# Kernel tuning notes

Measured on AMD Instinct MI355X. Metric: run time of the kernel, lower is better.

The kernel has to match this reference:

```python
import jax, jax.numpy as jnp
import numpy as np

# Dims: S strings, B batch, D bond dim, N=784 input sites, P=2 phys dim, L=10 labels
S, B, D, N, P, L = 4, 64, 32, 784, 2, 10
HALF = N // 2  # 392 sites on each side of the label node


def setup_inputs() -> dict:
    key = jax.random.key(0)
    ks = jax.random.split(key, 6)
    # scale chosen so each transfer-matrix step keeps vector norm ~O(1)
    std = (3.0 / (2.0 * D)) ** 0.5
    inputs = jax.random.uniform(ks[0], (B, N, P), dtype=jnp.float32)
    A_first = jax.random.normal(ks[1], (S, D, P), dtype=jnp.float32) * std          # node 0
    A_left = jax.random.normal(ks[2], (S, HALF - 1, D, P, D), dtype=jnp.float32) * std   # nodes 1..391
    A_label = jax.random.normal(ks[3], (S, D, L, D), dtype=jnp.float32) * std       # node 392 (open label edge)
    A_right = jax.random.normal(ks[4], (S, HALF - 1, D, P, D), dtype=jnp.float32) * std  # nodes 393..783
    A_last = jax.random.normal(ks[5], (S, D, P), dtype=jnp.float32) * std           # node 784
    return {"inputs": inputs, "A_first": A_first, "A_left": A_left,
            "A_label": A_label, "A_right": A_right, "A_last": A_last}


def reference(inputs, A_first, A_left, A_label, A_right, A_last):
    x = inputs  # (B, N, P); original reshapes each sample to (784, 2)
    # Contract physical legs with inputs -> per-site transfer matrices, site-major for scan
    Ml = jnp.einsum('snipj,bnp->nsbij', A_left, x[:, 1:HALF])      # (391, S, B, D, D)
    v0 = jnp.einsum('sdp,bp->sbd', A_first, x[:, 0])               # (S, B, D)

    def step_left(v, M):
        return jnp.einsum('sbi,sbij->sbj', v, M), None
    v, _ = jax.lax.scan(step_left, v0, Ml)                          # (S, B, D)

    T = jnp.einsum('sbd,sdlj->sblj', v, A_label)                    # (S, B, L, D)

    Mr = jnp.einsum('snipj,bnp->nsbij', A_right, x[:, HALF:N - 1])  # (391, S, B, D, D)
    r0 = jnp.einsum('sdp,bp->sbd', A_last, x[:, N - 1])             # (S, B, D)

    def step_right(r, M):
        return jnp.einsum('sbij,sbj->sbi', M, r), None
    r, _ = jax.lax.scan(step_right, r0, Mr, reverse=True)           # (S, B, D)

    out_per_string = jnp.einsum('sblj,sbj->sbl', T, r)              # (S, B, L)
    # forward multiplies the per-string 10-vectors elementwise (init ones)
    return jnp.prod(out_per_string, axis=0)                         # (B, L)
```

## Files before the change

kernel.cpp:

```cpp
#include <hip/hip_runtime.h>
#include <stdint.h>

#define S 4
#define B 64
#define D 32
#define N 784
#define P 2
#define L 10
#define HALF 392
#define NSTEP 391
#define NPAIR 196
#define SLICE 4096

typedef float f4 __attribute__((ext_vector_type(4)));

__device__ __forceinline__ float bcast(float v, int lane) {
    return __uint_as_float(__builtin_amdgcn_readlane(__float_as_uint(v), lane));
}

__global__ __launch_bounds__(256) void pair_kernel(
    const float* __restrict__ A_left, const float* __restrict__ A_right,
    float* __restrict__ Wbuf)
{
    const int t = blockIdx.x, stream = blockIdx.y;
    const int side = stream >> 2, s = stream & 3;
    __shared__ float sA[2048], sB[2048];
    const int tid = threadIdx.x;
    const bool leftover = (t == 195);

    const float* As = (side ? A_right : A_left) + (size_t)s * (NSTEP * 2048);
    int ia, ib;
    if (side == 0) { ia = 2 * t; ib = 2 * t + 1; }
    else           { ia = 389 - 2 * t; ib = 390 - 2 * t; }
    if (leftover)  { ia = side ? 0 : 390; ib = ia; }

    const float4* ga = (const float4*)(As + (size_t)ia * 2048);
    const float4* gb = (const float4*)(As + (size_t)ib * 2048);
    ((float4*)sA)[tid] = ga[tid]; ((float4*)sA)[tid + 256] = ga[tid + 256];
    ((float4*)sB)[tid] = gb[tid]; ((float4*)sB)[tid + 256] = gb[tid + 256];
    __syncthreads();

    const int c = tid >> 6, rest = tid & 63, ff = rest >> 1, eh = rest & 1;
    const int a = c & 1, bb = c >> 1;
    float out[16];

    if (!leftover) {
        if (side == 0) {
            float col[32];
            #pragma unroll
            for (int k = 0; k < 32; ++k) col[k] = sB[k * 64 + bb * 32 + ff];
            #pragma unroll
            for (int e0 = 0; e0 < 16; ++e0) {
                const int e = eh * 16 + e0; float acc = 0.f;
                #pragma unroll
                for (int k = 0; k < 32; ++k)
                    acc = fmaf(sA[e * 64 + a * 32 + k], col[k], acc);
                out[e0] = acc;
            }
        } else {
            float row[32];
            #pragma unroll
            for (int k = 0; k < 32; ++k) row[k] = sA[ff * 64 + a * 32 + k];
            #pragma unroll
            for (int e0 = 0; e0 < 16; ++e0) {
                const int e = eh * 16 + e0; float acc = 0.f;
                #pragma unroll
                for (int k = 0; k < 32; ++k)
                    acc = fmaf(row[k], sB[k * 64 + bb * 32 + e], acc);
                out[e0] = acc;
            }
        }
    } else {
        #pragma unroll
        for (int e0 = 0; e0 < 16; ++e0) {
            const int e = eh * 16 + e0;
            out[e0] = (side == 0) ? sA[e * 64 + a * 32 + ff]
                                  : sA[ff * 64 + a * 32 + e];
        }
    }

    float* Wt = Wbuf + ((size_t)stream * NPAIR + t) * SLICE;
    #pragma unroll
    for (int q0 = 0; q0 < 4; ++q0) {
        const int qq = eh * 4 + q0;
        float4 val = make_float4(out[q0 * 4 + 0], out[q0 * 4 + 1],
                                 out[q0 * 4 + 2], out[q0 * 4 + 3]);
        ((float4*)Wt)[(bb * 8 + qq) * 64 + a * 32 + ff] = val;
    }
}

__global__ __launch_bounds__(64) void wkern(const float* __restrict__ x,
                                            float* __restrict__ wtab)
{
    const int t = blockIdx.x, side = blockIdx.y, bb = threadIdx.x;
    const float2* x2 = (const float2*)x;
    float2 xa, xb;
    if (t < 195) {
        int na, nb;
        if (side == 0) { na = 2 * t + 1; nb = 2 * t + 2; }
        else           { int ma = 389 - 2 * t; na = HALF + ma; nb = na + 1; }
        xa = x2[(size_t)bb * N + na];
        xb = x2[(size_t)bb * N + nb];
    } else {
        const int na = side ? HALF : 391;
        xa = x2[(size_t)bb * N + na];
        xb = make_float2(1.f, 0.f);
    }
    float4 w = make_float4(xa.x * xb.x, xa.y * xb.x, xa.x * xb.y, xa.y * xb.y);
    ((float4*)wtab)[((size_t)side * NPAIR + t) * 64 + bb] = w;
}

#define GLOAD(dst, ptr, off) \
    asm volatile("global_load_dwordx4 %0, %1, off offset:" #off \
                 : "=v"(dst) : "v"(ptr))

#define ISSUE_SLOT(SL) do { \
    GLOAD(SL##0,  pA, 0); GLOAD(SL##1,  pA, 1024); GLOAD(SL##2,  pA, 2048); GLOAD(SL##3,  pA, 3072); \
    GLOAD(SL##4,  pB, 0); GLOAD(SL##5,  pB, 1024); GLOAD(SL##6,  pB, 2048); GLOAD(SL##7,  pB, 3072); \
    GLOAD(SL##8,  pC, 0); GLOAD(SL##9,  pC, 1024); GLOAD(SL##10, pC, 2048); GLOAD(SL##11, pC, 3072); \
    GLOAD(SL##12, pD, 0); GLOAD(SL##13, pD, 1024); GLOAD(SL##14, pD, 2048); GLOAD(SL##15, pD, 3072); \
    GLOAD(SL##w,  pw, 0); \
    pA += SLICE; pB += SLICE; pC += SLICE; pD += SLICE; pw += 256; \
} while (0)

#define WAIT(n) do { \
    asm volatile("s_waitcnt vmcnt(" #n ")"); \
    __builtin_amdgcn_sched_barrier(0); \
} while (0)

#define FMAQ(Rq, acc, eb) \
    acc = fmaf(Rq.x, bcast(v, eb + 0), acc); \
    acc = fmaf(Rq.y, bcast(v, eb + 1), acc); \
    acc = fmaf(Rq.z, bcast(v, eb + 2), acc); \
    acc = fmaf(Rq.w, bcast(v, eb + 3), acc);

#define CONSUME_SLOT(SL) do { \
    float a0 = 0.f, a1 = 0.f, a2 = 0.f, a3 = 0.f; \
    FMAQ(SL##0,  a0, 0)  FMAQ(SL##1,  a0, 4)  FMAQ(SL##2,  a0, 8)  FMAQ(SL##3,  a0, 12) \
    FMAQ(SL##4,  a1, 16) FMAQ(SL##5,  a1, 20) FMAQ(SL##6,  a1, 24) FMAQ(SL##7,  a1, 28) \
    FMAQ(SL##8,  a2, 0)  FMAQ(SL##9,  a2, 4)  FMAQ(SL##10, a2, 8)  FMAQ(SL##11, a2, 12) \
    FMAQ(SL##12, a3, 16) FMAQ(SL##13, a3, 20) FMAQ(SL##14, a3, 24) FMAQ(SL##15, a3, 28) \
    const float wlo = c2 ? SL##w.y : SL##w.x; \
    const float whi = c2 ? SL##w.w : SL##w.z; \
    const float part = fmaf(wlo, a0 + a1, whi * (a2 + a3)); \
    v = part + __shfl_xor(part, 32); \
} while (0)

__global__ __launch_bounds__(128, 1) void chain_kernel(
    const float* __restrict__ x,
    const float* __restrict__ A_first, const float* __restrict__ A_last,
    const float* __restrict__ Wbuf, const float* __restrict__ wtab,
    float* __restrict__ ws_v)
{
    const int tid = threadIdx.x, wv = tid >> 6, lane = tid & 63;
    const int c2 = lane >> 5, f = lane & 31;
    const int blk = blockIdx.x, stream = blk & 7;
    const int side = stream >> 2, s = stream & 3;
    const int b = (blk >> 3) * 2 + wv;

    const float2* x2 = (const float2*)x;
    float v;
    if (side == 0) {
        const float2 a  = ((const float2*)A_first)[s * D + f];
        const float2 xx = x2[(size_t)b * N + 0];
        v = fmaf(a.x, xx.x, a.y * xx.y);
    } else {
        const float2 a  = ((const float2*)A_last)[s * D + f];
        const float2 xx = x2[(size_t)b * N + (N - 1)];
        v = fmaf(a.x, xx.x, a.y * xx.y);
    }

    const float* Wstream = Wbuf + (size_t)stream * (NPAIR * SLICE);
    const float* pA = Wstream + (size_t)lane * 4;
    const float* pB = pA + 1024;
    const float* pC = pA + 2048;
    const float* pD = pA + 3072;
    const float* pw = wtab + ((size_t)side * NPAIR) * 256 + (size_t)b * 4;

    f4 A0,A1,A2,A3,A4,A5,A6,A7,A8,A9,A10,A11,A12,A13,A14,A15,Aw;
    f4 B0,B1,B2,B3,B4,B5,B6,B7,B8,B9,B10,B11,B12,B13,B14,B15,Bw;
    f4 C0,C1,C2,C3,C4,C5,C6,C7,C8,C9,C10,C11,C12,C13,C14,C15,Cw;

    ISSUE_SLOT(A);
    ISSUE_SLOT(B);

    for (int k = 0; k < 64; ++k) {
        ISSUE_SLOT(C); __builtin_amdgcn_s_barrier(); WAIT(34); CONSUME_SLOT(A);
        ISSUE_SLOT(A); __builtin_amdgcn_s_barrier(); WAIT(34); CONSUME_SLOT(B);
        ISSUE_SLOT(B); __builtin_amdgcn_s_barrier(); WAIT(34); CONSUME_SLOT(C);
    }
    ISSUE_SLOT(C);
    __builtin_amdgcn_s_barrier(); WAIT(34); CONSUME_SLOT(A);
    ISSUE_SLOT(A);
    __builtin_amdgcn_s_barrier(); WAIT(34); CONSUME_SLOT(B);
    __builtin_amdgcn_s_barrier(); WAIT(17); CONSUME_SLOT(C);
    __builtin_amdgcn_s_barrier(); WAIT(0);  CONSUME_SLOT(A);

    if (lane < 32)
        ws_v[(side * S + s) * (B * D) + b * D + f] = v;
}

__global__ __launch_bounds__(64) void chain_fb(
    const float* __restrict__ x, const float* __restrict__ A_first,
    const float* __restrict__ A_left, const float* __restrict__ A_right,
    const float* __restrict__ A_last, float* __restrict__ ws_v)
{
    const int blk = blockIdx.x, pair = blk & 7, b = blk >> 3;
    const int side = pair >> 2, s = pair & 3;
    const int lane = threadIdx.x, p = lane >> 5, j = lane & 31;
    const float* xb = x + b * (N * P);
    float v;
    if (side == 0) {
        v = fmaf(A_first[s*D*P + j*P + 0], xb[0], A_first[s*D*P + j*P + 1] * xb[1]);
        const float* Abase = A_left + (size_t)s * (NSTEP * D * P * D);
        for (int n = 1; n <= NSTEP; ++n) {
            const float* M = Abase + (n - 1) * (D * P * D) + p * D + j;
            const float x0 = xb[n*P], x1 = xb[n*P + 1];
            float t0 = 0.f, t1 = 0.f;
            #pragma unroll
            for (int i = 0; i < D; i += 2) {
                t0 = fmaf(bcast(v, i),     M[i * (P*D)],       t0);
                t1 = fmaf(bcast(v, i + 1), M[(i + 1) * (P*D)], t1);
            }
            const float t = t0 + t1, o = __shfl_xor(t, 32);
            v = (p == 0) ? fmaf(x0, t, x1 * o) : fmaf(x1, t, x0 * o);
        }
    } else {
        v = fmaf(A_last[s*D*P + j*P + 0], xb[(N-1)*P], A_last[s*D*P + j*P + 1] * xb[(N-1)*P + 1]);
        const float* Abase = A_right + (size_t)s * (NSTEP * D * P * D);
        for (int m = NSTEP - 1; m >= 0; --m) {
            const float4* R4 = (const float4*)(Abase + m * (D*P*D) + j * (P*D) + p * D);
            const float x0 = xb[(HALF+m)*P], x1 = xb[(HALF+m)*P + 1];
            float t0 = 0.f, t1 = 0.f;
            #pragma unroll
            for (int q = 0; q < 8; ++q) {
                const float4 rv = R4[q];
                t0 = fmaf(rv.x, bcast(v, 4*q+0), t0);
                t1 = fmaf(rv.y, bcast(v, 4*q+1), t1);
                t0 = fmaf(rv.z, bcast(v, 4*q+2), t0);
                t1 = fmaf(rv.w, bcast(v, 4*q+3), t1);
            }
            const float t = t0 + t1, o = __shfl_xor(t, 32);
            v = (p == 0) ? fmaf(x0, t, x1 * o) : fmaf(x1, t, x0 * o);
        }
    }
    if (p == 0) ws_v[(side*S + s)*(B*D) + b*D + j] = v;
}

__global__ __launch_bounds__(64) void label_kernel(
    const float* __restrict__ ws_v, const float* __restrict__ A_label,
    float* __restrict__ ws_o)
{
    const int blk = blockIdx.x, s = blk & 3, b = blk >> 2;
    const int lane = threadIdx.x, h = lane >> 5, j = lane & 31;
    const float vj = ws_v[(0*S + s)*(B*D) + b*D + j];
    const float rj = ws_v[(1*S + s)*(B*D) + b*D + j];
    #pragma unroll
    for (int q = 0; q < 5; ++q) {
        const int l = h * 5 + q;
        float w = 0.f;
        #pragma unroll
        for (int d = 0; d < D; ++d)
            w = fmaf(bcast(vj, d), A_label[((s*D + d)*L + l)*D + j], w);
        float c = w * rj;
        c += __shfl_xor(c, 1); c += __shfl_xor(c, 2); c += __shfl_xor(c, 4);
        c += __shfl_xor(c, 8); c += __shfl_xor(c, 16);
        if (j == 0) ws_o[(b*L + l)*S + s] = c;
    }
}

__global__ void prod_kernel(const float* __restrict__ ws_o, float* __restrict__ out) {
    const int t = blockIdx.x * blockDim.x + threadIdx.x;
    if (t < B * L) {
        const float* o = ws_o + t * S;
        out[t] = o[0] * o[1] * o[2] * o[3];
    }
}

extern "C" void kernel_launch(void* const* d_in, const int* in_sizes, int n_in,
                              void* d_out, int out_size, void* d_ws, size_t ws_size,
                              hipStream_t stream) {
    const float* x       = (const float*)d_in[0];
    const float* A_first = (const float*)d_in[1];
    const float* A_left  = (const float*)d_in[2];
    const float* A_label = (const float*)d_in[3];
    const float* A_right = (const float*)d_in[4];
    const float* A_last  = (const float*)d_in[5];
    float* out = (float*)d_out;

    float* ws_v = (float*)d_ws;
    float* ws_o = ws_v + 2 * S * B * D;
    float* wtab = ws_o + B * L * S;
    float* Wbuf = wtab + 2 * NPAIR * 64 * 4;
    const size_t need = (size_t)(16384 + 2560 + 100352 + 8 * NPAIR * SLICE) * 4;

    if (ws_size >= need) {
        pair_kernel<<<dim3(NPAIR, 8), dim3(256), 0, stream>>>(A_left, A_right, Wbuf);
        wkern<<<dim3(NPAIR, 2), dim3(64), 0, stream>>>(x, wtab);
        chain_kernel<<<dim3(256), dim3(128), 0, stream>>>(x, A_first, A_last, Wbuf, wtab, ws_v);
    } else {
        chain_fb<<<dim3(2 * S * B), dim3(64), 0, stream>>>(x, A_first, A_left, A_right, A_last, ws_v);
    }
    label_kernel<<<dim3(S * B), dim3(64), 0, stream>>>(ws_v, A_label, ws_o);
    prod_kernel<<<dim3((B * L + 255) / 256), dim3(256), 0, stream>>>(ws_o, out);
}
```

Before: 117.3 us.

## Process two batch rows per wave in chain kernel and fuse auxiliary kernels

The chain kernel now runs one 64-lane wave per block and handles two batch samples with the same loaded pair matrices, instead of two waves each loading the same data. This halves redundant global loads of the precomputed pair matrices and removes the inter-wave barriers, at the cost of more FMAs and registers per wave. The input-weight table computation moves into pair_kernel, and the label and product kernels are merged, which cuts two kernel launches.

```diff
diff --git a/kernel.cpp b/kernel.cpp
--- a/kernel.cpp
+++ b/kernel.cpp
@@ -20,10 +20,12 @@
 
 __global__ __launch_bounds__(256) void pair_kernel(
     const float* __restrict__ A_left, const float* __restrict__ A_right,
-    float* __restrict__ Wbuf)
+    const float* __restrict__ x,
+    float* __restrict__ Wbuf, float* __restrict__ wtab)
 {
-    const int t = blockIdx.x, stream = blockIdx.y;
-    const int side = stream >> 2, s = stream & 3;
+    const int stream = blockIdx.x;
+    const int t      = blockIdx.y;
+    const int side   = stream >> 2, s = stream & 3;
     __shared__ float sA[2048], sB[2048];
     const int tid = threadIdx.x;
     const bool leftover = (t == 195);
@@ -87,39 +89,36 @@
                                  out[q0 * 4 + 2], out[q0 * 4 + 3]);
         ((float4*)Wt)[(bb * 8 + qq) * 64 + a * 32 + ff] = val;
     }
-}
-
-__global__ __launch_bounds__(64) void wkern(const float* __restrict__ x,
-                                            float* __restrict__ wtab)
-{
-    const int t = blockIdx.x, side = blockIdx.y, bb = threadIdx.x;
-    const float2* x2 = (const float2*)x;
-    float2 xa, xb;
-    if (t < 195) {
-        int na, nb;
-        if (side == 0) { na = 2 * t + 1; nb = 2 * t + 2; }
-        else           { int ma = 389 - 2 * t; na = HALF + ma; nb = na + 1; }
-        xa = x2[(size_t)bb * N + na];
-        xb = x2[(size_t)bb * N + nb];
-    } else {
-        const int na = side ? HALF : 391;
-        xa = x2[(size_t)bb * N + na];
-        xb = make_float2(1.f, 0.f);
-    }
-    float4 w = make_float4(xa.x * xb.x, xa.y * xb.x, xa.x * xb.y, xa.y * xb.y);
-    ((float4*)wtab)[((size_t)side * NPAIR + t) * 64 + bb] = w;
-}
-
-#define GLOAD(dst, ptr, off) \
+
+    if (stream < 2 && tid < 64) {
+        const int sd = stream;
+        const float2* x2 = (const float2*)x;
+        float2 xa, xb;
+        if (!leftover) {
+            int na, nb;
+            if (sd == 0) { na = 2 * t + 1; nb = 2 * t + 2; }
+            else         { int ma = 389 - 2 * t; na = HALF + ma; nb = na + 1; }
+            xa = x2[(size_t)tid * N + na];
+            xb = x2[(size_t)tid * N + nb];
+        } else {
+            xa = x2[(size_t)tid * N + (sd ? HALF : 391)];
+            xb = make_float2(1.f, 0.f);
+        }
+        float4 w = make_float4(xa.x * xb.x, xa.y * xb.x, xa.x * xb.y, xa.y * xb.y);
+        ((float4*)wtab)[((size_t)sd * NPAIR + t) * 64 + tid] = w;
+    }
+}
+
+#define GLOAD4(dst, ptr, off) \
     asm volatile("global_load_dwordx4 %0, %1, off offset:" #off \
                  : "=v"(dst) : "v"(ptr))
 
 #define ISSUE_SLOT(SL) do { \
-    GLOAD(SL##0,  pA, 0); GLOAD(SL##1,  pA, 1024); GLOAD(SL##2,  pA, 2048); GLOAD(SL##3,  pA, 3072); \
-    GLOAD(SL##4,  pB, 0); GLOAD(SL##5,  pB, 1024); GLOAD(SL##6,  pB, 2048); GLOAD(SL##7,  pB, 3072); \
-    GLOAD(SL##8,  pC, 0); GLOAD(SL##9,  pC, 1024); GLOAD(SL##10, pC, 2048); GLOAD(SL##11, pC, 3072); \
-    GLOAD(SL##12, pD, 0); GLOAD(SL##13, pD, 1024); GLOAD(SL##14, pD, 2048); GLOAD(SL##15, pD, 3072); \
-    GLOAD(SL##w,  pw, 0); \
+    GLOAD4(SL##0,  pA, 0); GLOAD4(SL##1,  pA, 1024); GLOAD4(SL##2,  pA, 2048); GLOAD4(SL##3,  pA, 3072); \
+    GLOAD4(SL##4,  pB, 0); GLOAD4(SL##5,  pB, 1024); GLOAD4(SL##6,  pB, 2048); GLOAD4(SL##7,  pB, 3072); \
+    GLOAD4(SL##8,  pC, 0); GLOAD4(SL##9,  pC, 1024); GLOAD4(SL##10, pC, 2048); GLOAD4(SL##11, pC, 3072); \
+    GLOAD4(SL##12, pD, 0); GLOAD4(SL##13, pD, 1024); GLOAD4(SL##14, pD, 2048); GLOAD4(SL##15, pD, 3072); \
+    GLOAD4(SL##w0, pw, 0); GLOAD4(SL##w1, pw, 16); \
     pA += SLICE; pB += SLICE; pC += SLICE; pD += SLICE; pw += 256; \
 } while (0)
 
@@ -128,76 +127,85 @@
     __builtin_amdgcn_sched_barrier(0); \
 } while (0)
 
-#define FMAQ(Rq, acc, eb) \
-    acc = fmaf(Rq.x, bcast(v, eb + 0), acc); \
-    acc = fmaf(Rq.y, bcast(v, eb + 1), acc); \
-    acc = fmaf(Rq.z, bcast(v, eb + 2), acc); \
-    acc = fmaf(Rq.w, bcast(v, eb + 3), acc);
+#define FMAD2_1(RL_, RH_, aL0, aH0, aL1, aH1, E) do { \
+    const float s_ = bcast(v0, E), t_ = bcast(v1, E); \
+    aL0 = fmaf(RL_, s_, aL0); aH0 = fmaf(RH_, s_, aH0); \
+    aL1 = fmaf(RL_, t_, aL1); aH1 = fmaf(RH_, t_, aH1); \
+} while (0)
+
+#define FMAD2(RqL, RqH, aL0, aH0, aL1, aH1, eb) \
+    FMAD2_1(RqL.x, RqH.x, aL0, aH0, aL1, aH1, eb + 0); \
+    FMAD2_1(RqL.y, RqH.y, aL0, aH0, aL1, aH1, eb + 1); \
+    FMAD2_1(RqL.z, RqH.z, aL0, aH0, aL1, aH1, eb + 2); \
+    FMAD2_1(RqL.w, RqH.w, aL0, aH0, aL1, aH1, eb + 3);
 
 #define CONSUME_SLOT(SL) do { \
-    float a0 = 0.f, a1 = 0.f, a2 = 0.f, a3 = 0.f; \
-    FMAQ(SL##0,  a0, 0)  FMAQ(SL##1,  a0, 4)  FMAQ(SL##2,  a0, 8)  FMAQ(SL##3,  a0, 12) \
-    FMAQ(SL##4,  a1, 16) FMAQ(SL##5,  a1, 20) FMAQ(SL##6,  a1, 24) FMAQ(SL##7,  a1, 28) \
-    FMAQ(SL##8,  a2, 0)  FMAQ(SL##9,  a2, 4)  FMAQ(SL##10, a2, 8)  FMAQ(SL##11, a2, 12) \
-    FMAQ(SL##12, a3, 16) FMAQ(SL##13, a3, 20) FMAQ(SL##14, a3, 24) FMAQ(SL##15, a3, 28) \
-    const float wlo = c2 ? SL##w.y : SL##w.x; \
-    const float whi = c2 ? SL##w.w : SL##w.z; \
-    const float part = fmaf(wlo, a0 + a1, whi * (a2 + a3)); \
-    v = part + __shfl_xor(part, 32); \
+    float q00 = 0.f, q01 = 0.f, q02 = 0.f, q03 = 0.f; \
+    float q10 = 0.f, q11 = 0.f, q12 = 0.f, q13 = 0.f; \
+    FMAD2(SL##0, SL##8,  q00, q02, q10, q12, 0)  \
+    FMAD2(SL##1, SL##9,  q00, q02, q10, q12, 4)  \
+    FMAD2(SL##2, SL##10, q00, q02, q10, q12, 8)  \
+    FMAD2(SL##3, SL##11, q00, q02, q10, q12, 12) \
+    FMAD2(SL##4, SL##12, q01, q03, q11, q13, 16) \
+    FMAD2(SL##5, SL##13, q01, q03, q11, q13, 20) \
+    FMAD2(SL##6, SL##14, q01, q03, q11, q13, 24) \
+    FMAD2(SL##7, SL##15, q01, q03, q11, q13, 28) \
+    const float wl0 = c2 ? SL##w0.y : SL##w0.x, wh0 = c2 ? SL##w0.w : SL##w0.z; \
+    const float wl1 = c2 ? SL##w1.y : SL##w1.x, wh1 = c2 ? SL##w1.w : SL##w1.z; \
+    const float part0 = fmaf(wl0, q00 + q01, wh0 * (q02 + q03)); \
+    const float part1 = fmaf(wl1, q10 + q11, wh1 * (q12 + q13)); \
+    v0 = part0 + __shfl_xor(part0, 32); \
+    v1 = part1 + __shfl_xor(part1, 32); \
 } while (0)
 
-__global__ __launch_bounds__(128, 1) void chain_kernel(
+__global__ __launch_bounds__(64, 1) void chain_kernel(
     const float* __restrict__ x,
     const float* __restrict__ A_first, const float* __restrict__ A_last,
     const float* __restrict__ Wbuf, const float* __restrict__ wtab,
     float* __restrict__ ws_v)
 {
-    const int tid = threadIdx.x, wv = tid >> 6, lane = tid & 63;
-    const int c2 = lane >> 5, f = lane & 31;
+    const int lane = threadIdx.x, c2 = lane >> 5, f = lane & 31;
     const int blk = blockIdx.x, stream = blk & 7;
     const int side = stream >> 2, s = stream & 3;
-    const int b = (blk >> 3) * 2 + wv;
+    const int bp = blk >> 3;
+    const int b0 = 2 * bp, b1 = 2 * bp + 1;
 
     const float2* x2 = (const float2*)x;
-    float v;
-    if (side == 0) {
-        const float2 a  = ((const float2*)A_first)[s * D + f];
-        const float2 xx = x2[(size_t)b * N + 0];
-        v = fmaf(a.x, xx.x, a.y * xx.y);
-    } else {
-        const float2 a  = ((const float2*)A_last)[s * D + f];
-        const float2 xx = x2[(size_t)b * N + (N - 1)];
-        v = fmaf(a.x, xx.x, a.y * xx.y);
-    }
+    const int site0 = side ? (N - 1) : 0;
+    const float2 af  = ((const float2*)(side ? A_last : A_first))[s * D + f];
+    const float2 xx0 = x2[(size_t)b0 * N + site0];
+    const float2 xx1 = x2[(size_t)b1 * N + site0];
+    float v0 = fmaf(af.x, xx0.x, af.y * xx0.y);
+    float v1 = fmaf(af.x, xx1.x, af.y * xx1.y);
 
     const float* Wstream = Wbuf + (size_t)stream * (NPAIR * SLICE);
     const float* pA = Wstream + (size_t)lane * 4;
     const float* pB = pA + 1024;
     const float* pC = pA + 2048;
     const float* pD = pA + 3072;
-    const float* pw = wtab + ((size_t)side * NPAIR) * 256 + (size_t)b * 4;
-
-    f4 A0,A1,A2,A3,A4,A5,A6,A7,A8,A9,A10,A11,A12,A13,A14,A15,Aw;
-    f4 B0,B1,B2,B3,B4,B5,B6,B7,B8,B9,B10,B11,B12,B13,B14,B15,Bw;
-    f4 C0,C1,C2,C3,C4,C5,C6,C7,C8,C9,C10,C11,C12,C13,C14,C15,Cw;
+    const float* pw = wtab + (((size_t)side * NPAIR) * 64 + 2 * bp) * 4;
+
+    f4 A0,A1,A2,A3,A4,A5,A6,A7,A8,A9,A10,A11,A12,A13,A14,A15,Aw0,Aw1;
+    f4 B0,B1,B2,B3,B4,B5,B6,B7,B8,B9,B10,B11,B12,B13,B14,B15,Bw0,Bw1;
+    f4 C0,C1,C2,C3,C4,C5,C6,C7,C8,C9,C10,C11,C12,C13,C14,C15,Cw0,Cw1;
 
     ISSUE_SLOT(A);
     ISSUE_SLOT(B);
 
     for (int k = 0; k < 64; ++k) {
-        ISSUE_SLOT(C); __builtin_amdgcn_s_barrier(); WAIT(34); CONSUME_SLOT(A);
-        ISSUE_SLOT(A); __builtin_amdgcn_s_barrier(); WAIT(34); CONSUME_SLOT(B);
-        ISSUE_SLOT(B); __builtin_amdgcn_s_barrier(); WAIT(34); CONSUME_SLOT(C);
-    }
-    ISSUE_SLOT(C);
-    __builtin_amdgcn_s_barrier(); WAIT(34); CONSUME_SLOT(A);
-    ISSUE_SLOT(A);
-    __builtin_amdgcn_s_barrier(); WAIT(34); CONSUME_SLOT(B);
-    __builtin_amdgcn_s_barrier(); WAIT(17); CONSUME_SLOT(C);
-    __builtin_amdgcn_s_barrier(); WAIT(0);  CONSUME_SLOT(A);
-
-    if (lane < 32)
-        ws_v[(side * S + s) * (B * D) + b * D + f] = v;
+        ISSUE_SLOT(C); WAIT(36); CONSUME_SLOT(A);
+        ISSUE_SLOT(A); WAIT(36); CONSUME_SLOT(B);
+        ISSUE_SLOT(B); WAIT(36); CONSUME_SLOT(C);
+    }
+    ISSUE_SLOT(C); WAIT(36); CONSUME_SLOT(A);
+    ISSUE_SLOT(A); WAIT(36); CONSUME_SLOT(B);
+    WAIT(18); CONSUME_SLOT(C);
+    WAIT(0);  CONSUME_SLOT(A);
+
+    if (lane < 32) {
+        ws_v[(side * S + s) * (B * D) + b0 * D + f] = v0;
+        ws_v[(side * S + s) * (B * D) + b1 * D + f] = v1;
+    }
 }
 
 __global__ __launch_bounds__(64) void chain_fb(
@@ -247,33 +255,38 @@
     if (p == 0) ws_v[(side*S + s)*(B*D) + b*D + j] = v;
 }
 
-__global__ __launch_bounds__(64) void label_kernel(
+__global__ __launch_bounds__(64) void label_prod_kernel(
     const float* __restrict__ ws_v, const float* __restrict__ A_label,
-    float* __restrict__ ws_o)
+    float* __restrict__ out)
 {
-    const int blk = blockIdx.x, s = blk & 3, b = blk >> 2;
+    const int b = blockIdx.x;
     const int lane = threadIdx.x, h = lane >> 5, j = lane & 31;
-    const float vj = ws_v[(0*S + s)*(B*D) + b*D + j];
-    const float rj = ws_v[(1*S + s)*(B*D) + b*D + j];
+    float pr0 = 1.f, pr1 = 1.f, pr2 = 1.f, pr3 = 1.f, pr4 = 1.f;
+
     #pragma unroll
-    for (int q = 0; q < 5; ++q) {
-        const int l = h * 5 + q;
-        float w = 0.f;
+    for (int s = 0; s < S; ++s) {
+        const float vj = ws_v[(0 * S + s) * (B * D) + b * D + j];
+        const float rj = ws_v[(1 * S + s) * (B * D) + b * D + j];
         #pragma unroll
-        for (int d = 0; d < D; ++d)
-            w = fmaf(bcast(vj, d), A_label[((s*D + d)*L + l)*D + j], w);
-        float c = w * rj;
-        c += __shfl_xor(c, 1); c += __shfl_xor(c, 2); c += __shfl_xor(c, 4);
-        c += __shfl_xor(c, 8); c += __shfl_xor(c, 16);
-        if (j == 0) ws_o[(b*L + l)*S + s] = c;
-    }
-}
-
-__global__ void prod_kernel(const float* __restrict__ ws_o, float* __restrict__ out) {
-    const int t = blockIdx.x * blockDim.x + threadIdx.x;
-    if (t < B * L) {
-        const float* o = ws_o + t * S;
-        out[t] = o[0] * o[1] * o[2] * o[3];
+        for (int q = 0; q < 5; ++q) {
+            const int l = h * 5 + q;
+            float w = 0.f;
+            #pragma unroll
+            for (int d = 0; d < D; ++d)
+                w = fmaf(bcast(vj, d), A_label[((s * D + d) * L + l) * D + j], w);
+            float c = w * rj;
+            c += __shfl_xor(c, 1); c += __shfl_xor(c, 2); c += __shfl_xor(c, 4);
+            c += __shfl_xor(c, 8); c += __shfl_xor(c, 16);
+            if (q == 0) pr0 *= c; else if (q == 1) pr1 *= c;
+            else if (q == 2) pr2 *= c; else if (q == 3) pr3 *= c; else pr4 *= c;
+        }
+    }
+    if (j == 0) {
+        out[b * L + h * 5 + 0] = pr0;
+        out[b * L + h * 5 + 1] = pr1;
+        out[b * L + h * 5 + 2] = pr2;
+        out[b * L + h * 5 + 3] = pr3;
+        out[b * L + h * 5 + 4] = pr4;
     }
 }
 
@@ -289,18 +302,15 @@
     float* out = (float*)d_out;
 
     float* ws_v = (float*)d_ws;
-    float* ws_o = ws_v + 2 * S * B * D;
-    float* wtab = ws_o + B * L * S;
+    float* wtab = ws_v + 2 * S * B * D;
     float* Wbuf = wtab + 2 * NPAIR * 64 * 4;
-    const size_t need = (size_t)(16384 + 2560 + 100352 + 8 * NPAIR * SLICE) * 4;
+    const size_t need = (size_t)(16384 + 100352 + 8 * NPAIR * SLICE) * 4;
 
     if (ws_size >= need) {
-        pair_kernel<<<dim3(NPAIR, 8), dim3(256), 0, stream>>>(A_left, A_right, Wbuf);
-        wkern<<<dim3(NPAIR, 2), dim3(64), 0, stream>>>(x, wtab);
-        chain_kernel<<<dim3(256), dim3(128), 0, stream>>>(x, A_first, A_last, Wbuf, wtab, ws_v);
+        pair_kernel<<<dim3(8, NPAIR), dim3(256), 0, stream>>>(A_left, A_right, x, Wbuf, wtab);
+        chain_kernel<<<dim3(256), dim3(64), 0, stream>>>(x, A_first, A_last, Wbuf, wtab, ws_v);
     } else {
         chain_fb<<<dim3(2 * S * B), dim3(64), 0, stream>>>(x, A_first, A_left, A_right, A_last, ws_v);
     }
-    label_kernel<<<dim3(S * B), dim3(64), 0, stream>>>(ws_v, A_label, ws_o);
-    prod_kernel<<<dim3((B * L + 255) / 256), dim3(256), 0, stream>>>(ws_o, out);
-}
+    label_prod_kernel<<<dim3(B), dim3(64), 0, stream>>>(ws_v, A_label, out);
+}
```

Measured after the change: 124.2 us. 5.9% more time.
